# Optimization experiments

Measured on AMD Instinct MI355X. Metric: run time of the kernel, lower is better.

The kernel has to match this reference:

```python
import jax, jax.numpy as jnp
import numpy as np

N_NODES = 50000
N_EDGES = 150000
N_REL = 65
N_GRAPHS = 2000
F_IN = 74
H = 256
M_H = 64


def _rel_norm(dst, etype):
    # PyG RGCNConv default aggr='mean': mean over incoming edges per (node, relation)
    comb = dst * N_REL + etype
    cnt = jax.ops.segment_sum(jnp.ones(dst.shape[0], jnp.float32), comb,
                              num_segments=N_NODES * N_REL)
    return 1.0 / jnp.maximum(cnt[comb], 1.0)  # [E]


def rgcn_conv(x, src, dst, etype, norm, W, W_root, b):
    # x: [N, Fin]; W: [R, Fin, Fout]; out: [N, Fout]
    msg = x[src] * norm[:, None]  # [E, Fin]

    def step(out, wr):
        W_r, r = wr
        m = (etype == r)[:, None]
        agg = jax.ops.segment_sum(jnp.where(m, msg, 0.0), dst,
                                  num_segments=N_NODES)  # [N, Fin]
        return out + agg @ W_r, None

    out0 = x @ W_root + b
    out, _ = jax.lax.scan(step, out0, (W, jnp.arange(N_REL)))
    return out


def setup_inputs() -> dict:
    key = jax.random.key(0)
    ks = jax.random.split(key, 20)
    s = 0.05
    inp = {
        "x": jax.random.normal(ks[0], (N_NODES, F_IN), jnp.float32),
        "edge_index": jax.random.randint(ks[1], (2, N_EDGES), 0, N_NODES, jnp.int32),
        "edge_type": jax.random.randint(ks[2], (N_EDGES,), 0, N_REL, jnp.int32),
        "batch": jnp.sort(jax.random.randint(ks[3], (N_NODES,), 0, N_GRAPHS, jnp.int32)),
        # RGCN layer 1
        "W1": jax.random.normal(ks[4], (N_REL, F_IN, H), jnp.float32) * s,
        "root1": jax.random.normal(ks[5], (F_IN, H), jnp.float32) * s,
        "b1": jnp.zeros((H,), jnp.float32),
        # RGCN layer 2
        "W2": jax.random.normal(ks[6], (N_REL, H, H), jnp.float32) * s,
        "root2": jax.random.normal(ks[7], (H, H), jnp.float32) * s,
        "b2": jnp.zeros((H,), jnp.float32),
        # WeightedSum gate
        "ws_w": jax.random.normal(ks[8], (H, 1), jnp.float32) * s,
        "ws_b": jnp.zeros((1,), jnp.float32),
        # MLP head 256 -> 64 -> 64 -> 1
        "m1": jax.random.normal(ks[9], (H, M_H), jnp.float32) * s,
        "mb1": jnp.zeros((M_H,), jnp.float32),
        "m2": jax.random.normal(ks[10], (M_H, M_H), jnp.float32) * s,
        "mb2": jnp.zeros((M_H,), jnp.float32),
        "m3": jax.random.normal(ks[11], (M_H, 1), jnp.float32) * s,
        "mb3": jnp.zeros((1,), jnp.float32),
    }
    return inp


def reference(x, edge_index, edge_type, batch,
              W1, root1, b1, W2, root2, b2,
              ws_w, ws_b, m1, mb1, m2, mb2, m3, mb3):
    src, dst = edge_index[0], edge_index[1]
    norm = _rel_norm(dst, edge_type)

    h = jax.nn.relu(rgcn_conv(x, src, dst, edge_type, norm, W1, root1, b1))
    h = jax.nn.relu(rgcn_conv(h, src, dst, edge_type, norm, W2, root2, b2))
    # dropout is identity in eval mode

    # WeightedSum pooling over graphs
    w = jax.nn.sigmoid(h @ ws_w + ws_b)  # [N, 1]
    g = jax.ops.segment_sum(w * h, batch, num_segments=N_GRAPHS)  # [G, H]

    # MLP head (eval: dropout off; default batch-norm with unit stats ~ identity)
    g = jax.nn.relu(g @ m1 + mb1)
    g = jax.nn.relu(g @ m2 + mb2)
    return g @ m3 + mb3  # [G, 1]
```

## Files before the change

### kernel.cpp

```cpp
#include <hip/hip_runtime.h>
#include <hip/hip_bf16.h>

#define NN 50000
#define NE 150000
#define NR 65
#define NG 2000
#define FIN 74
#define KP 96
#define HD 256
#define MH 64

#define TE2 128
#define MAX_T2 20

#define EPB 1024
#define NB ((NE + EPB - 1) / EPB)
#define NTOT (NR * NB)

#define SCHUNK 512

typedef __attribute__((ext_vector_type(8))) short bf16x8;
typedef __attribute__((ext_vector_type(4))) float f32x4;

__device__ __forceinline__ unsigned short f2bf(float x) {
  unsigned u = __builtin_bit_cast(unsigned, x);
  u += 0x7FFF + ((u >> 16) & 1);
  return (unsigned short)(u >> 16);
}
__device__ __forceinline__ float bf2f(unsigned short h) {
  unsigned u = (unsigned)h << 16;
  return __builtin_bit_cast(float, u);
}

__device__ __forceinline__ void gl16(const short* g, short* lds) {
  __builtin_amdgcn_global_load_lds(
      (const __attribute__((address_space(1))) void*)g,
      (__attribute__((address_space(3))) void*)lds, 16, 0, 0);
}

__global__ void build_wt(const float* __restrict__ Wsrc, short* __restrict__ dst,
                         int Kin, int KC, int nmat) {
  int tid = blockIdx.x * 256 + threadIdx.x;
  int total = nmat * 2 * KC * 512;
  if (tid >= total) return;
  int c = tid & 3;
  int colin = (tid >> 2) & 15;
  int grp = (tid >> 6) & 7;
  int rem = tid >> 9;
  int ks = rem % KC;  rem /= KC;
  int half = rem & 1;
  int mat = rem >> 1;
  int col = half * 128 + grp * 16 + colin;
  bf16x8 hv, lv;
#pragma unroll
  for (int i = 0; i < 8; ++i) {
    int kk = (i < 4) ? (c * 4 + i) : (16 + c * 4 + (i - 4));
    int k = ks * 32 + kk;
    float v = (k < Kin) ? Wsrc[((size_t)mat * Kin + k) * HD + col] : 0.f;
    unsigned short h = f2bf(v);
    hv[i] = (short)h;
    lv[i] = (short)f2bf(v - bf2f(h));
  }
  int byteoff = grp * 1024 + ((colin * 64 + c * 16) ^ ((colin & 7) << 4));
  char* basehi = (char*)dst + ((size_t)((mat * 2 + half) * 2 + 0) * KC) * 8192;
  char* baselo = (char*)dst + ((size_t)((mat * 2 + half) * 2 + 1) * KC) * 8192;
  *(bf16x8*)(basehi + (size_t)ks * 8192 + byteoff) = hv;
  *(bf16x8*)(baselo + (size_t)ks * 8192 + byteoff) = lv;
}

__global__ void padx_k(const float* __restrict__ x, float* __restrict__ xp) {
  int i = blockIdx.x * 256 + threadIdx.x;
  if (i < NN * KP) {
    int n = i / KP, k = i - n * KP;
    xp[i] = (k < FIN) ? x[(size_t)n * FIN + k] : 0.f;
  }
}

__global__ void count_k(const int* __restrict__ dst, const int* __restrict__ et,
                        int* __restrict__ cnt, int* __restrict__ ndeg) {
  int e = blockIdx.x * 256 + threadIdx.x;
  if (e < NE) {
    atomicAdd(&cnt[(size_t)dst[e] * NR + et[e]], 1);
    atomicAdd(&ndeg[dst[e]], 1);
  }
}

__global__ void gcount_k(const int* __restrict__ batch, int* __restrict__ ghist) {
  int i = blockIdx.x * 256 + threadIdx.x;
  if (i < NN) atomicAdd(&ghist[batch[i]], 1);
}

__global__ __launch_bounds__(EPB) void histblk_k(const int* __restrict__ et,
                                                 int* __restrict__ bh) {
  __shared__ int lh[NR];
  int t = threadIdx.x, b = blockIdx.x;
  if (t < NR) lh[t] = 0;
  __syncthreads();
  int e = b * EPB + t;
  if (e < NE) atomicAdd(&lh[et[e]], 1);
  __syncthreads();
  if (t < NR) bh[t * NB + b] = lh[t];
}

__global__ __launch_bounds__(256) void psum_k(const int* __restrict__ in,
                                              int* __restrict__ bsum, int n) {
  __shared__ int ws4[4];
  int b = blockIdx.x, t = threadIdx.x;
  int base = b * SCHUNK;
  int s = 0;
#pragma unroll
  for (int i = 0; i < SCHUNK / 256; ++i) {
    int g = base + t + i * 256;
    if (g < n) s += in[g];
  }
#pragma unroll
  for (int o = 32; o > 0; o >>= 1) s += __shfl_down(s, o, 64);
  if ((t & 63) == 0) ws4[t >> 6] = s;
  __syncthreads();
  if (t == 0) bsum[b] = ws4[0] + ws4[1] + ws4[2] + ws4[3];
}

__global__ __launch_bounds__(256) void scanb_k(int* __restrict__ bsum, int nb) {
  __shared__ int ld[256];
  int t = threadIdx.x;
  int v = (t < nb) ? bsum[t] : 0;
  ld[t] = v;
  __syncthreads();
  int acc = v;
#pragma unroll
  for (int o = 1; o < 256; o <<= 1) {
    int u = (t >= o) ? ld[t - o] : 0;
    __syncthreads();
    acc += u;
    ld[t] = acc;
    __syncthreads();
  }
  if (t < nb) bsum[t] = acc - v;
  if (t == nb - 1) bsum[nb] = acc;
}

__global__ __launch_bounds__(256) void apply_k(const int* __restrict__ in,
                                               const int* __restrict__ bsum,
                                               int* __restrict__ out, int n) {
  __shared__ int ld[256];
  int b = blockIdx.x, t = threadIdx.x;
  int base = b * SCHUNK + t * 2;
  int v0 = (base < n) ? in[base] : 0;
  int v1 = (base + 1 < n) ? in[base + 1] : 0;
  int ps = v0 + v1;
  ld[t] = ps;
  __syncthreads();
  int acc = ps;
#pragma unroll
  for (int o = 1; o < 256; o <<= 1) {
    int u = (t >= o) ? ld[t - o] : 0;
    __syncthreads();
    acc += u;
    ld[t] = acc;
    __syncthreads();
  }
  int excl = acc - ps + bsum[b];
  if (base < n) out[base] = excl;
  if (base + 1 < n) out[base + 1] = excl + v0;
  if (base == n - 1) out[n] = excl + v0;
  else if (base + 1 == n - 1) out[n] = excl + v0 + v1;
}

__global__ void offr_k(const int* __restrict__ start, int* __restrict__ offr) {
  int t = threadIdx.x;
  if (t < NR) offr[t] = start[t * NB];
  if (t == NR) offr[NR] = start[NTOT];
}

__global__ __launch_bounds__(EPB) void place_k(const int* __restrict__ src,
                                               const int* __restrict__ dst,
                                               const int* __restrict__ et,
                                               const int* __restrict__ cnt,
                                               const int* __restrict__ start,
                                               int* __restrict__ es,
                                               int* __restrict__ ed,
                                               float* __restrict__ enorm) {
  __shared__ int lcur[NR];
  int t = threadIdx.x, b = blockIdx.x;
  if (t < NR) lcur[t] = 0;
  __syncthreads();
  int e = b * EPB + t;
  if (e < NE) {
    int r = et[e];
    int d = dst[e];
    int rank = atomicAdd(&lcur[r], 1);
    int p = start[r * NB + b] + rank;
    es[p] = src[e];
    ed[p] = d;
    int c = cnt[(size_t)d * NR + r];
    enorm[p] = 1.0f / (float)(c > 0 ? c : 1);
  }
}

__global__ void plist_k(const int* __restrict__ ed, const int* __restrict__ nodeoff,
                        int* __restrict__ ncur, int* __restrict__ plist) {
  int p = blockIdx.x * 256 + threadIdx.x;
  if (p < NE) {
    int d = ed[p];
    int q = nodeoff[d] + atomicAdd(&ncur[d], 1);
    plist[q] = p;
  }
}

#define MFMA_BF16 __builtin_amdgcn_mfma_f32_16x16x32_bf16

template<int K>
__global__ __launch_bounds__(256) void gemm_edge(const float* __restrict__ X,
                                                 const short* __restrict__ Wt,
                                                 const int* __restrict__ es,
                                                 const float* __restrict__ enorm,
                                                 const int* __restrict__ offr,
                                                 float* __restrict__ tmp,
                                                 int half) {
  constexpr int KC = K / 32;
  __shared__ __align__(16) short Ah[4096], Al[4096], Bh[4096], Bl[4096];
  const int t = threadIdx.x;
  const int rel = blockIdx.x / MAX_T2;
  const int tile = blockIdx.x % MAX_T2;
  const int e_lo = offr[rel], e_hi = offr[rel + 1];
  if (e_lo + tile * TE2 >= e_hi) return;
  const short* WtM = Wt + (size_t)(rel * 2 + half) * (2 * KC * 4096);
  const int lane = t & 63, wv = t >> 6;
  const int r = t & 127, cp = t >> 7;
  const int rowb = (wv & 1) * 64, colb = (wv >> 1) * 64;
  const int fo = (((lane & 15) * 64 + (lane >> 4) * 16) ^ ((lane & 7) << 4)) >> 1;

  for (int base = e_lo + tile * TE2; base < e_hi; base += MAX_T2 * TE2) {
    const int nE = min(TE2, e_hi - base);
    const float* xrow = X + (size_t)es[base + ((r < nE) ? r : 0)] * K;
    const float nrm = (r < nE) ? enorm[base + r] : 0.f;
    f32x4 acc[4][4];
#pragma unroll
    for (int f = 0; f < 4; ++f)
#pragma unroll
      for (int n = 0; n < 4; ++n) acc[f][n] = {0.f, 0.f, 0.f, 0.f};

    for (int ks = 0; ks < KC; ++ks) {
#pragma unroll
      for (int j = 0; j < 2; ++j) {
        int ch = wv * 2 + j;
        gl16(WtM + (size_t)ks * 4096 + ch * 512 + lane * 8, &Bh[ch * 512]);
        gl16(WtM + (size_t)(KC + ks) * 4096 + ch * 512 + lane * 8, &Bl[ch * 512]);
      }
#pragma unroll
      for (int j = 0; j < 2; ++j) {
        int c = cp * 2 + j;
        float4 a = *(const float4*)&xrow[ks * 32 + c * 4];
        float4 b = *(const float4*)&xrow[ks * 32 + 16 + c * 4];
        float v[8] = {a.x * nrm, a.y * nrm, a.z * nrm, a.w * nrm,
                      b.x * nrm, b.y * nrm, b.z * nrm, b.w * nrm};
        bf16x8 hv, lv;
#pragma unroll
        for (int i = 0; i < 8; ++i) {
          unsigned short h = f2bf(v[i]);
          hv[i] = (short)h;
          lv[i] = (short)f2bf(v[i] - bf2f(h));
        }
        int ab = (r * 64 + c * 16) ^ ((r & 7) << 4);
        *(bf16x8*)((char*)Ah + ab) = hv;
        *(bf16x8*)((char*)Al + ab) = lv;
      }
      __syncthreads();
      bf16x8 afh[4], afl[4], bfh[4], bfl[4];
#pragma unroll
      for (int f = 0; f < 4; ++f) {
        int o = (rowb + f * 16) * 32 + fo;
        afh[f] = *(const bf16x8*)&Ah[o];
        afl[f] = *(const bf16x8*)&Al[o];
      }
#pragma unroll
      for (int n = 0; n < 4; ++n) {
        int o = (colb + n * 16) * 32 + fo;
        bfh[n] = *(const bf16x8*)&Bh[o];
        bfl[n] = *(const bf16x8*)&Bl[o];
      }
#pragma unroll
      for (int f = 0; f < 4; ++f)
#pragma unroll
        for (int n = 0; n < 4; ++n) {
          acc[f][n] = MFMA_BF16(afh[f], bfh[n], acc[f][n], 0, 0, 0);
          acc[f][n] = MFMA_BF16(afh[f], bfl[n], acc[f][n], 0, 0, 0);
          acc[f][n] = MFMA_BF16(afl[f], bfh[n], acc[f][n], 0, 0, 0);
        }
      __syncthreads();
    }
#pragma unroll
    for (int f = 0; f < 4; ++f) {
      int rb = rowb + f * 16 + (lane >> 4) * 4;
#pragma unroll
      for (int rr = 0; rr < 4; ++rr) {
        int row = rb + rr;
        if (row < nE) {
          float* o = &tmp[(size_t)(base + row) * 128 + colb + (lane & 15)];
#pragma unroll
          for (int n = 0; n < 4; ++n) o[n * 16] = acc[f][n][rr];
        }
      }
    }
  }
}

template<int K>
__global__ __launch_bounds__(256) void gemm_root(const float* __restrict__ X,
                                                 const short* __restrict__ Wtr,
                                                 const float* __restrict__ bias,
                                                 float* __restrict__ out, int M) {
  constexpr int KC = K / 32;
  __shared__ __align__(16) short Ah[4096], Al[4096], Bh[4096], Bl[4096];
  const int t = threadIdx.x;
  const int row0 = blockIdx.x * TE2;
  const int half = blockIdx.y;
  const short* WtM = Wtr + (size_t)half * (2 * KC * 4096);
  const int lane = t & 63, wv = t >> 6;
  const int r = t & 127, cp = t >> 7;
  const int rowb = (wv & 1) * 64, colb = (wv >> 1) * 64;
  const int fo = (((lane & 15) * 64 + (lane >> 4) * 16) ^ ((lane & 7) << 4)) >> 1;

  const int gr = row0 + r;
  const float* xrow = X + (size_t)(gr < M ? gr : 0) * K;
  const float nrm = (gr < M) ? 1.f : 0.f;
  f32x4 acc[4][4];
#pragma unroll
  for (int f = 0; f < 4; ++f)
#pragma unroll
    for (int n = 0; n < 4; ++n) acc[f][n] = {0.f, 0.f, 0.f, 0.f};

  for (int ks = 0; ks < KC; ++ks) {
#pragma unroll
    for (int j = 0; j < 2; ++j) {
      int ch = wv * 2 + j;
      gl16(WtM + (size_t)ks * 4096 + ch * 512 + lane * 8, &Bh[ch * 512]);
      gl16(WtM + (size_t)(KC + ks) * 4096 + ch * 512 + lane * 8, &Bl[ch * 512]);
    }
#pragma unroll
    for (int j = 0; j < 2; ++j) {
      int c = cp * 2 + j;
      float4 a = *(const float4*)&xrow[ks * 32 + c * 4];
      float4 b = *(const float4*)&xrow[ks * 32 + 16 + c * 4];
      float v[8] = {a.x * nrm, a.y * nrm, a.z * nrm, a.w * nrm,
                    b.x * nrm, b.y * nrm, b.z * nrm, b.w * nrm};
      bf16x8 hv, lv;
#pragma unroll
      for (int i = 0; i < 8; ++i) {
        unsigned short h = f2bf(v[i]);
        hv[i] = (short)h;
        lv[i] = (short)f2bf(v[i] - bf2f(h));
      }
      int ab = (r * 64 + c * 16) ^ ((r & 7) << 4);
      *(bf16x8*)((char*)Ah + ab) = hv;
      *(bf16x8*)((char*)Al + ab) = lv;
    }
    __syncthreads();
    bf16x8 afh[4], afl[4], bfh[4], bfl[4];
#pragma unroll
    for (int f = 0; f < 4; ++f) {
      int o = (rowb + f * 16) * 32 + fo;
      afh[f] = *(const bf16x8*)&Ah[o];
      afl[f] = *(const bf16x8*)&Al[o];
    }
#pragma unroll
    for (int n = 0; n < 4; ++n) {
      int o = (colb + n * 16) * 32 + fo;
      bfh[n] = *(const bf16x8*)&Bh[o];
      bfl[n] = *(const bf16x8*)&Bl[o];
    }
#pragma unroll
    for (int f = 0; f < 4; ++f)
#pragma unroll
      for (int n = 0; n < 4; ++n) {
        acc[f][n] = MFMA_BF16(afh[f], bfh[n], acc[f][n], 0, 0, 0);
        acc[f][n] = MFMA_BF16(afh[f], bfl[n], acc[f][n], 0, 0, 0);
        acc[f][n] = MFMA_BF16(afl[f], bfh[n], acc[f][n], 0, 0, 0);
      }
    __syncthreads();
  }
#pragma unroll
  for (int f = 0; f < 4; ++f) {
    int rb = rowb + f * 16 + (lane >> 4) * 4;
#pragma unroll
    for (int rr = 0; rr < 4; ++rr) {
      int row = rb + rr;
      if (row0 + row < M) {
#pragma unroll
        for (int n = 0; n < 4; ++n) {
          int cg = half * 128 + colb + n * 16 + (lane & 15);
          out[(size_t)(row0 + row) * HD + cg] = acc[f][n][rr] + bias[cg];
        }
      }
    }
  }
}

__global__ __launch_bounds__(256) void reduce_k(float* __restrict__ h,
                                                const float* __restrict__ tmp,
                                                const int* __restrict__ nodeoff,
                                                const int* __restrict__ plist,
                                                int col0) {
  int wid = (blockIdx.x * 256 + threadIdx.x) >> 6;
  int lane = threadIdx.x & 63;
  if (wid >= NN) return;
  float* row = h + (size_t)wid * HD + col0 + lane * 2;
  float2 acc = *(float2*)row;
  int lo = nodeoff[wid], hi = nodeoff[wid + 1];
  for (int q = lo; q < hi; ++q) {
    int p = plist[q];
    float2 v = *(const float2*)&tmp[(size_t)p * 128 + lane * 2];
    acc.x += v.x; acc.y += v.y;
  }
  acc.x = fmaxf(acc.x, 0.f);
  acc.y = fmaxf(acc.y, 0.f);
  *(float2*)row = acc;
}

__global__ __launch_bounds__(256) void pool_k(const float* __restrict__ h,
                                              const float* __restrict__ wsw,
                                              const float* __restrict__ wsb,
                                              const int* __restrict__ goff,
                                              float* __restrict__ g) {
  int wid = (blockIdx.x * 256 + threadIdx.x) >> 6;
  int lane = threadIdx.x & 63;
  if (wid >= NG) return;
  float4 w4 = *(const float4*)&wsw[lane * 4];
  float wb = wsb[0];
  float4 acc = make_float4(0.f, 0.f, 0.f, 0.f);
  int lo = goff[wid], hi = goff[wid + 1];
  for (int n = lo; n < hi; ++n) {
    float4 v = *(const float4*)&h[(size_t)n * HD + lane * 4];
    float p = v.x * w4.x + v.y * w4.y + v.z * w4.z + v.w * w4.w;
#pragma unroll
    for (int o = 32; o > 0; o >>= 1) p += __shfl_xor(p, o, 64);
    float gate = 1.f / (1.f + expf(-(p + wb)));
    acc.x += gate * v.x;
    acc.y += gate * v.y;
    acc.z += gate * v.z;
    acc.w += gate * v.w;
  }
  *(float4*)&g[(size_t)wid * HD + lane * 4] = acc;
}

__global__ __launch_bounds__(64) void mlp_k(const float* __restrict__ g,
                                            const float* __restrict__ m1,
                                            const float* __restrict__ mb1,
                                            const float* __restrict__ m2,
                                            const float* __restrict__ mb2,
                                            const float* __restrict__ m3,
                                            const float* __restrict__ mb3,
                                            float* __restrict__ out) {
  __shared__ float sg[HD];
  __shared__ float s1[MH];
  int gr = blockIdx.x;
  int t = threadIdx.x;
  float4 v = *(const float4*)&g[(size_t)gr * HD + t * 4];
  *(float4*)&sg[t * 4] = v;
  __syncthreads();
  float a = mb1[t];
  for (int k = 0; k < HD; ++k) a += sg[k] * m1[k * MH + t];
  a = fmaxf(a, 0.f);
  s1[t] = a;
  __syncthreads();
  float b = mb2[t];
#pragma unroll
  for (int k = 0; k < MH; ++k) b += s1[k] * m2[k * MH + t];
  b = fmaxf(b, 0.f);
  float c = b * m3[t];
#pragma unroll
  for (int o = 32; o > 0; o >>= 1) c += __shfl_xor(c, o, 64);
  if (t == 0) out[gr] = c + mb3[0];
}

extern "C" void kernel_launch(void* const* d_in, const int* in_sizes, int n_in,
                              void* d_out, int out_size, void* d_ws, size_t ws_size,
                              hipStream_t stream) {
  const float* x = (const float*)d_in[0];
  const int* ei = (const int*)d_in[1];
  const int* etype = (const int*)d_in[2];
  const int* batch = (const int*)d_in[3];
  const float* W1 = (const float*)d_in[4];
  const float* root1 = (const float*)d_in[5];
  const float* b1 = (const float*)d_in[6];
  const float* W2 = (const float*)d_in[7];
  const float* root2 = (const float*)d_in[8];
  const float* b2 = (const float*)d_in[9];
  const float* wsw = (const float*)d_in[10];
  const float* wsb = (const float*)d_in[11];
  const float* m1 = (const float*)d_in[12];
  const float* mb1 = (const float*)d_in[13];
  const float* m2 = (const float*)d_in[14];
  const float* mb2 = (const float*)d_in[15];
  const float* m3 = (const float*)d_in[16];
  const float* mb3 = (const float*)d_in[17];
  const int* esrc = ei;
  const int* edst = ei + NE;

  constexpr int KC1 = KP / 32;
  constexpr int KC2 = HD / 32;
  const int nbN = (NN + SCHUNK - 1) / SCHUNK;
  const int nbT = (NTOT + SCHUNK - 1) / SCHUNK;
  const int nbG = (NG + SCHUNK - 1) / SCHUNK;

  char* ws = (char*)d_ws;
  size_t off = 0;
  auto alloc = [&](size_t bytes) {
    size_t o = off;
    off = (off + bytes + 255) & ~(size_t)255;
    return o;
  };
  size_t o_tmp = alloc((size_t)NE * 128 * 4);
  size_t o_h1 = alloc((size_t)NN * HD * 4);
  size_t o_h2x = alloc((size_t)NN * HD * 4);
  size_t o_g = alloc((size_t)NG * HD * 4);
  size_t o_es = alloc((size_t)NE * 4);
  size_t o_ed = alloc((size_t)NE * 4);
  size_t o_enorm = alloc((size_t)NE * 4);
  size_t o_plist = alloc((size_t)NE * 4);
  size_t o_nodeoff = alloc((NN + 1) * 4);
  size_t o_goff = alloc((NG + 1) * 4);
  size_t o_offr = alloc((NR + 1) * 4);
  size_t o_bh = alloc((size_t)NTOT * 4);
  size_t o_start = alloc((size_t)(NTOT + 1) * 4);
  size_t o_bsN = alloc((size_t)(nbN + 1) * 4);
  size_t o_bsT = alloc((size_t)(nbT + 1) * 4);
  size_t o_bsG = alloc((size_t)(nbG + 1) * 4);
  size_t o_wt2 = alloc((size_t)NR * 4 * KC2 * 4096 * 2);
  size_t o_wtr2 = alloc((size_t)4 * KC2 * 4096 * 2);
  size_t zs = off;
  size_t o_ndeg = alloc((size_t)NN * 4);
  size_t o_ncur = alloc((size_t)NN * 4);
  size_t o_ghist = alloc((size_t)NG * 4);
  size_t ze = off;
  if (ws_size < off) return;

  float* tmp = (float*)(ws + o_tmp);
  int* cnt = (int*)(ws + o_tmp);
  float* h1 = (float*)(ws + o_h1);
  float* h2 = (float*)(ws + o_h2x);
  float* xp = (float*)(ws + o_h2x);
  short* wt1 = (short*)(ws + o_h2x + 19200000);
  short* wtr1 = (short*)(ws + o_h2x + 19200000 + 6389760);
  float* g = (float*)(ws + o_g);
  int* es = (int*)(ws + o_es);
  int* ed = (int*)(ws + o_ed);
  float* enorm = (float*)(ws + o_enorm);
  int* plist = (int*)(ws + o_plist);
  int* nodeoff = (int*)(ws + o_nodeoff);
  int* goff = (int*)(ws + o_goff);
  int* offr = (int*)(ws + o_offr);
  int* bh = (int*)(ws + o_bh);
  int* start = (int*)(ws + o_start);
  int* bsN = (int*)(ws + o_bsN);
  int* bsT = (int*)(ws + o_bsT);
  int* bsG = (int*)(ws + o_bsG);
  short* wt2 = (short*)(ws + o_wt2);
  short* wtr2 = (short*)(ws + o_wtr2);
  int* ndeg = (int*)(ws + o_ndeg);
  int* ncur = (int*)(ws + o_ncur);
  int* ghist = (int*)(ws + o_ghist);
  float* outp = (float*)d_out;

  hipMemsetAsync(ws + o_tmp, 0, (size_t)NN * NR * 4, stream);
  hipMemsetAsync(ws + zs, 0, ze - zs, stream);

  padx_k<<<(NN * KP + 255) / 256, 256, 0, stream>>>(x, xp);
  build_wt<<<(NR * 2 * KC1 * 512 + 255) / 256, 256, 0, stream>>>(W1, wt1, FIN, KC1, NR);
  build_wt<<<(2 * KC1 * 512 + 255) / 256, 256, 0, stream>>>(root1, wtr1, FIN, KC1, 1);
  build_wt<<<(NR * 2 * KC2 * 512 + 255) / 256, 256, 0, stream>>>(W2, wt2, HD, KC2, NR);
  build_wt<<<(2 * KC2 * 512 + 255) / 256, 256, 0, stream>>>(root2, wtr2, HD, KC2, 1);

  count_k<<<(NE + 255) / 256, 256, 0, stream>>>(edst, etype, cnt, ndeg);
  gcount_k<<<(NN + 255) / 256, 256, 0, stream>>>(batch, ghist);
  histblk_k<<<NB, EPB, 0, stream>>>(etype, bh);

  psum_k<<<nbT, 256, 0, stream>>>(bh, bsT, NTOT);
  scanb_k<<<1, 256, 0, stream>>>(bsT, nbT);
  apply_k<<<nbT, 256, 0, stream>>>(bh, bsT, start, NTOT);
  offr_k<<<1, 128, 0, stream>>>(start, offr);

  psum_k<<<nbN, 256, 0, stream>>>(ndeg, bsN, NN);
  scanb_k<<<1, 256, 0, stream>>>(bsN, nbN);
  apply_k<<<nbN, 256, 0, stream>>>(ndeg, bsN, nodeoff, NN);

  psum_k<<<nbG, 256, 0, stream>>>(ghist, bsG, NG);
  scanb_k<<<1, 256, 0, stream>>>(bsG, nbG);
  apply_k<<<nbG, 256, 0, stream>>>(ghist, bsG, goff, NG);

  place_k<<<NB, EPB, 0, stream>>>(esrc, edst, etype, cnt, start, es, ed, enorm);
  plist_k<<<(NE + 255) / 256, 256, 0, stream>>>(ed, nodeoff, ncur, plist);

  const dim3 gRoot((NN + TE2 - 1) / TE2, 2);
  const int gEdge = NR * MAX_T2;
  const int nRed = (NN * 64 + 255) / 256;

  gemm_root<KP><<<gRoot, 256, 0, stream>>>(xp, wtr1, b1, h1, NN);
  gemm_edge<KP><<<gEdge, 256, 0, stream>>>(xp, wt1, es, enorm, offr, tmp, 0);
  reduce_k<<<nRed, 256, 0, stream>>>(h1, tmp, nodeoff, plist, 0);
  gemm_edge<KP><<<gEdge, 256, 0, stream>>>(xp, wt1, es, enorm, offr, tmp, 1);
  reduce_k<<<nRed, 256, 0, stream>>>(h1, tmp, nodeoff, plist, 128);

  gemm_root<HD><<<gRoot, 256, 0, stream>>>(h1, wtr2, b2, h2, NN);
  gemm_edge<HD><<<gEdge, 256, 0, stream>>>(h1, wt2, es, enorm, offr, tmp, 0);
  reduce_k<<<nRed, 256, 0, stream>>>(h2, tmp, nodeoff, plist, 0);
  gemm_edge<HD><<<gEdge, 256, 0, stream>>>(h1, wt2, es, enorm, offr, tmp, 1);
  reduce_k<<<nRed, 256, 0, stream>>>(h2, tmp, nodeoff, plist, 128);

  pool_k<<<(NG * 64 + 255) / 256, 256, 0, stream>>>(h2, wsw, wsb, goff, g);
  mlp_k<<<NG, 64, 0, stream>>>(g, m1, mb1, m2, mb2, m3, mb3, outp);
}
```

Baseline: 588.2 us.

## Compute full 256-wide output per block and store edge messages in bf16

The edge and root GEMMs now use 512-thread blocks that cover all 256 output columns in one pass, instead of two launches over 128-column halves. Each edge row's gathered features are loaded and split once rather than twice, and the reduce kernel runs once per layer. The per-edge intermediate buffer is stored as bf16 instead of fp32, halving its write and read traffic. The cost is larger LDS use per block and rounding of the per-edge messages to bf16 before accumulation.

```diff
diff --git a/kernel.cpp b/kernel.cpp
--- a/kernel.cpp
+++ b/kernel.cpp
@@ -41,16 +41,15 @@
 __global__ void build_wt(const float* __restrict__ Wsrc, short* __restrict__ dst,
                          int Kin, int KC, int nmat) {
   int tid = blockIdx.x * 256 + threadIdx.x;
-  int total = nmat * 2 * KC * 512;
+  int total = nmat * KC * 1024;
   if (tid >= total) return;
   int c = tid & 3;
   int colin = (tid >> 2) & 15;
-  int grp = (tid >> 6) & 7;
-  int rem = tid >> 9;
-  int ks = rem % KC;  rem /= KC;
-  int half = rem & 1;
-  int mat = rem >> 1;
-  int col = half * 128 + grp * 16 + colin;
+  int grp = (tid >> 6) & 15;
+  int rem = tid >> 10;
+  int ks = rem % KC;
+  int mat = rem / KC;
+  int col = grp * 16 + colin;
   bf16x8 hv, lv;
 #pragma unroll
   for (int i = 0; i < 8; ++i) {
@@ -61,11 +60,10 @@
     hv[i] = (short)h;
     lv[i] = (short)f2bf(v - bf2f(h));
   }
-  int byteoff = grp * 1024 + ((colin * 64 + c * 16) ^ ((colin & 7) << 4));
-  char* basehi = (char*)dst + ((size_t)((mat * 2 + half) * 2 + 0) * KC) * 8192;
-  char* baselo = (char*)dst + ((size_t)((mat * 2 + half) * 2 + 1) * KC) * 8192;
-  *(bf16x8*)(basehi + (size_t)ks * 8192 + byteoff) = hv;
-  *(bf16x8*)(baselo + (size_t)ks * 8192 + byteoff) = lv;
+  int slot = grp * 1024 + ((colin * 64 + c * 16) ^ ((colin & 7) << 4));
+  size_t matbase = (size_t)mat * 2 * KC * 16384;
+  *(bf16x8*)((char*)dst + matbase + (size_t)ks * 16384 + slot) = hv;
+  *(bf16x8*)((char*)dst + matbase + (size_t)(KC + ks) * 16384 + slot) = lv;
 }
 
 __global__ void padx_k(const float* __restrict__ x, float* __restrict__ xp) {
@@ -210,24 +208,24 @@
 #define MFMA_BF16 __builtin_amdgcn_mfma_f32_16x16x32_bf16
 
 template<int K>
-__global__ __launch_bounds__(256) void gemm_edge(const float* __restrict__ X,
+__global__ __launch_bounds__(512) void gemm_edge(const float* __restrict__ X,
                                                  const short* __restrict__ Wt,
                                                  const int* __restrict__ es,
                                                  const float* __restrict__ enorm,
                                                  const int* __restrict__ offr,
-                                                 float* __restrict__ tmp,
-                                                 int half) {
+                                                 unsigned short* __restrict__ tmp) {
   constexpr int KC = K / 32;
-  __shared__ __align__(16) short Ah[4096], Al[4096], Bh[4096], Bl[4096];
+  __shared__ __align__(16) short Ah[4096], Al[4096], Bh[8192], Bl[8192];
   const int t = threadIdx.x;
   const int rel = blockIdx.x / MAX_T2;
   const int tile = blockIdx.x % MAX_T2;
   const int e_lo = offr[rel], e_hi = offr[rel + 1];
   if (e_lo + tile * TE2 >= e_hi) return;
-  const short* WtM = Wt + (size_t)(rel * 2 + half) * (2 * KC * 4096);
-  const int lane = t & 63, wv = t >> 6;
-  const int r = t & 127, cp = t >> 7;
-  const int rowb = (wv & 1) * 64, colb = (wv >> 1) * 64;
+  const short* WtM = Wt + (size_t)rel * (2 * KC * 8192);
+  const int lane = t & 63, w = t >> 6;
+  const int r = t & 127, c = t >> 7;
+  const int rowg = (w & 1) * 4;
+  const int colg = (w >> 1) * 4;
   const int fo = (((lane & 15) * 64 + (lane >> 4) * 16) ^ ((lane & 7) << 4)) >> 1;
 
   for (int base = e_lo + tile * TE2; base < e_hi; base += MAX_T2 * TE2) {
@@ -243,13 +241,11 @@
     for (int ks = 0; ks < KC; ++ks) {
 #pragma unroll
       for (int j = 0; j < 2; ++j) {
-        int ch = wv * 2 + j;
-        gl16(WtM + (size_t)ks * 4096 + ch * 512 + lane * 8, &Bh[ch * 512]);
-        gl16(WtM + (size_t)(KC + ks) * 4096 + ch * 512 + lane * 8, &Bl[ch * 512]);
-      }
-#pragma unroll
-      for (int j = 0; j < 2; ++j) {
-        int c = cp * 2 + j;
+        int ch = w * 2 + j;
+        gl16(WtM + (size_t)ks * 8192 + ch * 512 + lane * 8, &Bh[ch * 512]);
+        gl16(WtM + (size_t)(KC + ks) * 8192 + ch * 512 + lane * 8, &Bl[ch * 512]);
+      }
+      {
         float4 a = *(const float4*)&xrow[ks * 32 + c * 4];
         float4 b = *(const float4*)&xrow[ks * 32 + 16 + c * 4];
         float v[8] = {a.x * nrm, a.y * nrm, a.z * nrm, a.w * nrm,
@@ -269,13 +265,13 @@
       bf16x8 afh[4], afl[4], bfh[4], bfl[4];
 #pragma unroll
       for (int f = 0; f < 4; ++f) {
-        int o = (rowb + f * 16) * 32 + fo;
+        int o = (rowg + f) * 512 + fo;
         afh[f] = *(const bf16x8*)&Ah[o];
         afl[f] = *(const bf16x8*)&Al[o];
       }
 #pragma unroll
       for (int n = 0; n < 4; ++n) {
-        int o = (colb + n * 16) * 32 + fo;
+        int o = (colg + n) * 512 + fo;
         bfh[n] = *(const bf16x8*)&Bh[o];
         bfl[n] = *(const bf16x8*)&Bl[o];
       }
@@ -291,14 +287,14 @@
     }
 #pragma unroll
     for (int f = 0; f < 4; ++f) {
-      int rb = rowb + f * 16 + (lane >> 4) * 4;
+      int rb = (rowg + f) * 16 + (lane >> 4) * 4;
 #pragma unroll
       for (int rr = 0; rr < 4; ++rr) {
         int row = rb + rr;
         if (row < nE) {
-          float* o = &tmp[(size_t)(base + row) * 128 + colb + (lane & 15)];
-#pragma unroll
-          for (int n = 0; n < 4; ++n) o[n * 16] = acc[f][n][rr];
+          unsigned short* o = &tmp[(size_t)(base + row) * HD + colg * 16 + (lane & 15)];
+#pragma unroll
+          for (int n = 0; n < 4; ++n) o[n * 16] = f2bf(acc[f][n][rr]);
         }
       }
     }
@@ -306,19 +302,18 @@
 }
 
 template<int K>
-__global__ __launch_bounds__(256) void gemm_root(const float* __restrict__ X,
+__global__ __launch_bounds__(512) void gemm_root(const float* __restrict__ X,
                                                  const short* __restrict__ Wtr,
                                                  const float* __restrict__ bias,
                                                  float* __restrict__ out, int M) {
   constexpr int KC = K / 32;
-  __shared__ __align__(16) short Ah[4096], Al[4096], Bh[4096], Bl[4096];
+  __shared__ __align__(16) short Ah[4096], Al[4096], Bh[8192], Bl[8192];
   const int t = threadIdx.x;
   const int row0 = blockIdx.x * TE2;
-  const int half = blockIdx.y;
-  const short* WtM = Wtr + (size_t)half * (2 * KC * 4096);
-  const int lane = t & 63, wv = t >> 6;
-  const int r = t & 127, cp = t >> 7;
-  const int rowb = (wv & 1) * 64, colb = (wv >> 1) * 64;
+  const int lane = t & 63, w = t >> 6;
+  const int r = t & 127, c = t >> 7;
+  const int rowg = (w & 1) * 4;
+  const int colg = (w >> 1) * 4;
   const int fo = (((lane & 15) * 64 + (lane >> 4) * 16) ^ ((lane & 7) << 4)) >> 1;
 
   const int gr = row0 + r;
@@ -333,13 +328,11 @@
   for (int ks = 0; ks < KC; ++ks) {
 #pragma unroll
     for (int j = 0; j < 2; ++j) {
-      int ch = wv * 2 + j;
-      gl16(WtM + (size_t)ks * 4096 + ch * 512 + lane * 8, &Bh[ch * 512]);
-      gl16(WtM + (size_t)(KC + ks) * 4096 + ch * 512 + lane * 8, &Bl[ch * 512]);
+      int ch = w * 2 + j;
+      gl16(Wtr + (size_t)ks * 8192 + ch * 512 + lane * 8, &Bh[ch * 512]);
+      gl16(Wtr + (size_t)(KC + ks) * 8192 + ch * 512 + lane * 8, &Bl[ch * 512]);
     }
-#pragma unroll
-    for (int j = 0; j < 2; ++j) {
-      int c = cp * 2 + j;
+    {
       float4 a = *(const float4*)&xrow[ks * 32 + c * 4];
       float4 b = *(const float4*)&xrow[ks * 32 + 16 + c * 4];
       float v[8] = {a.x * nrm, a.y * nrm, a.z * nrm, a.w * nrm,
@@ -359,13 +352,13 @@
     bf16x8 afh[4], afl[4], bfh[4], bfl[4];
 #pragma unroll
     for (int f = 0; f < 4; ++f) {
-      int o = (rowb + f * 16) * 32 + fo;
+      int o = (rowg + f) * 512 + fo;
       afh[f] = *(const bf16x8*)&Ah[o];
       afl[f] = *(const bf16x8*)&Al[o];
     }
 #pragma unroll
     for (int n = 0; n < 4; ++n) {
-      int o = (colb + n * 16) * 32 + fo;
+      int o = (colg + n) * 512 + fo;
       bfh[n] = *(const bf16x8*)&Bh[o];
       bfl[n] = *(const bf16x8*)&Bl[o];
     }
@@ -381,14 +374,14 @@
   }
 #pragma unroll
   for (int f = 0; f < 4; ++f) {
-    int rb = rowb + f * 16 + (lane >> 4) * 4;
+    int rb = (rowg + f) * 16 + (lane >> 4) * 4;
 #pragma unroll
     for (int rr = 0; rr < 4; ++rr) {
       int row = rb + rr;
       if (row0 + row < M) {
 #pragma unroll
         for (int n = 0; n < 4; ++n) {
-          int cg = half * 128 + colb + n * 16 + (lane & 15);
+          int cg = (colg + n) * 16 + (lane & 15);
           out[(size_t)(row0 + row) * HD + cg] = acc[f][n][rr] + bias[cg];
         }
       }
@@ -397,24 +390,28 @@
 }
 
 __global__ __launch_bounds__(256) void reduce_k(float* __restrict__ h,
-                                                const float* __restrict__ tmp,
+                                                const unsigned short* __restrict__ tmp,
                                                 const int* __restrict__ nodeoff,
-                                                const int* __restrict__ plist,
-                                                int col0) {
+                                                const int* __restrict__ plist) {
   int wid = (blockIdx.x * 256 + threadIdx.x) >> 6;
   int lane = threadIdx.x & 63;
   if (wid >= NN) return;
-  float* row = h + (size_t)wid * HD + col0 + lane * 2;
-  float2 acc = *(float2*)row;
+  float* row = h + (size_t)wid * HD + lane * 4;
+  float4 acc = *(float4*)row;
   int lo = nodeoff[wid], hi = nodeoff[wid + 1];
   for (int q = lo; q < hi; ++q) {
     int p = plist[q];
-    float2 v = *(const float2*)&tmp[(size_t)p * 128 + lane * 2];
-    acc.x += v.x; acc.y += v.y;
+    ushort4 m = *(const ushort4*)&tmp[(size_t)p * HD + lane * 4];
+    acc.x += bf2f(m.x);
+    acc.y += bf2f(m.y);
+    acc.z += bf2f(m.z);
+    acc.w += bf2f(m.w);
   }
   acc.x = fmaxf(acc.x, 0.f);
   acc.y = fmaxf(acc.y, 0.f);
-  *(float2*)row = acc;
+  acc.z = fmaxf(acc.z, 0.f);
+  acc.w = fmaxf(acc.w, 0.f);
+  *(float4*)row = acc;
 }
 
 __global__ __launch_bounds__(256) void pool_k(const float* __restrict__ h,
@@ -510,7 +507,7 @@
     off = (off + bytes + 255) & ~(size_t)255;
     return o;
   };
-  size_t o_tmp = alloc((size_t)NE * 128 * 4);
+  size_t o_tmp = alloc((size_t)NE * HD * 2);
   size_t o_h1 = alloc((size_t)NN * HD * 4);
   size_t o_h2x = alloc((size_t)NN * HD * 4);
   size_t o_g = alloc((size_t)NG * HD * 4);
@@ -526,8 +523,8 @@
   size_t o_bsN = alloc((size_t)(nbN + 1) * 4);
   size_t o_bsT = alloc((size_t)(nbT + 1) * 4);
   size_t o_bsG = alloc((size_t)(nbG + 1) * 4);
-  size_t o_wt2 = alloc((size_t)NR * 4 * KC2 * 4096 * 2);
-  size_t o_wtr2 = alloc((size_t)4 * KC2 * 4096 * 2);
+  size_t o_wt2 = alloc((size_t)NR * 2 * KC2 * 16384);
+  size_t o_wtr2 = alloc((size_t)2 * KC2 * 16384);
   size_t zs = off;
   size_t o_ndeg = alloc((size_t)NN * 4);
   size_t o_ncur = alloc((size_t)NN * 4);
@@ -535,7 +532,7 @@
   size_t ze = off;
   if (ws_size < off) return;
 
-  float* tmp = (float*)(ws + o_tmp);
+  unsigned short* tmp = (unsigned short*)(ws + o_tmp);
   int* cnt = (int*)(ws + o_tmp);
   float* h1 = (float*)(ws + o_h1);
   float* h2 = (float*)(ws + o_h2x);
@@ -566,10 +563,10 @@
   hipMemsetAsync(ws + zs, 0, ze - zs, stream);
 
   padx_k<<<(NN * KP + 255) / 256, 256, 0, stream>>>(x, xp);
-  build_wt<<<(NR * 2 * KC1 * 512 + 255) / 256, 256, 0, stream>>>(W1, wt1, FIN, KC1, NR);
-  build_wt<<<(2 * KC1 * 512 + 255) / 256, 256, 0, stream>>>(root1, wtr1, FIN, KC1, 1);
-  build_wt<<<(NR * 2 * KC2 * 512 + 255) / 256, 256, 0, stream>>>(W2, wt2, HD, KC2, NR);
-  build_wt<<<(2 * KC2 * 512 + 255) / 256, 256, 0, stream>>>(root2, wtr2, HD, KC2, 1);
+  build_wt<<<(NR * KC1 * 1024 + 255) / 256, 256, 0, stream>>>(W1, wt1, FIN, KC1, NR);
+  build_wt<<<(KC1 * 1024 + 255) / 256, 256, 0, stream>>>(root1, wtr1, FIN, KC1, 1);
+  build_wt<<<(NR * KC2 * 1024 + 255) / 256, 256, 0, stream>>>(W2, wt2, HD, KC2, NR);
+  build_wt<<<(KC2 * 1024 + 255) / 256, 256, 0, stream>>>(root2, wtr2, HD, KC2, 1);
 
   count_k<<<(NE + 255) / 256, 256, 0, stream>>>(edst, etype, cnt, ndeg);
   gcount_k<<<(NN + 255) / 256, 256, 0, stream>>>(batch, ghist);
@@ -591,21 +588,17 @@
   place_k<<<NB, EPB, 0, stream>>>(esrc, edst, etype, cnt, start, es, ed, enorm);
   plist_k<<<(NE + 255) / 256, 256, 0, stream>>>(ed, nodeoff, ncur, plist);
 
-  const dim3 gRoot((NN + TE2 - 1) / TE2, 2);
+  const int gRoot = (NN + TE2 - 1) / TE2;
   const int gEdge = NR * MAX_T2;
   const int nRed = (NN * 64 + 255) / 256;
 
-  gemm_root<KP><<<gRoot, 256, 0, stream>>>(xp, wtr1, b1, h1, NN);
-  gemm_edge<KP><<<gEdge, 256, 0, stream>>>(xp, wt1, es, enorm, offr, tmp, 0);
-  reduce_k<<<nRed, 256, 0, stream>>>(h1, tmp, nodeoff, plist, 0);
-  gemm_edge<KP><<<gEdge, 256, 0, stream>>>(xp, wt1, es, enorm, offr, tmp, 1);
-  reduce_k<<<nRed, 256, 0, stream>>>(h1, tmp, nodeoff, plist, 128);
-
-  gemm_root<HD><<<gRoot, 256, 0, stream>>>(h1, wtr2, b2, h2, NN);
-  gemm_edge<HD><<<gEdge, 256, 0, stream>>>(h1, wt2, es, enorm, offr, tmp, 0);
-  reduce_k<<<nRed, 256, 0, stream>>>(h2, tmp, nodeoff, plist, 0);
-  gemm_edge<HD><<<gEdge, 256, 0, stream>>>(h1, wt2, es, enorm, offr, tmp, 1);
-  reduce_k<<<nRed, 256, 0, stream>>>(h2, tmp, nodeoff, plist, 128);
+  gemm_root<KP><<<gRoot, 512, 0, stream>>>(xp, wtr1, b1, h1, NN);
+  gemm_edge<KP><<<gEdge, 512, 0, stream>>>(xp, wt1, es, enorm, offr, tmp);
+  reduce_k<<<nRed, 256, 0, stream>>>(h1, tmp, nodeoff, plist);
+
+  gemm_root<HD><<<gRoot, 512, 0, stream>>>(h1, wtr2, b2, h2, NN);
+  gemm_edge<HD><<<gEdge, 512, 0, stream>>>(h1, wt2, es, enorm, offr, tmp);
+  reduce_k<<<nRed, 256, 0, stream>>>(h2, tmp, nodeoff, plist);
 
   pool_k<<<(NG * 64 + 255) / 256, 256, 0, stream>>>(h2, wsw, wsb, goff, g);
   mlp_k<<<NG, 64, 0, stream>>>(g, m1, mb1, m2, mb2, m3, mb3, outp);
```

After: 546.8 us. -7.0%, faster.
